# Kernel optimization log

Measured on AMD Instinct MI355X. Metric: run time of the kernel, lower is better.

Reference implementation:

```python
import jax, jax.numpy as jnp
import numpy as np

B, L, D, H = 2, 2048, 2048, 16
DH = D // H  # head dim = 128
NEG = -1e9


def setup_inputs() -> dict:
    key = jax.random.key(0)
    ks = jax.random.split(key, 8)
    scale = 1.0 / np.sqrt(D)
    x = jax.random.normal(ks[0], (B, L, D), jnp.float32)
    # causal additive mask, broadcast over batch and heads
    causal = jnp.tril(jnp.ones((L, L), jnp.float32))
    mask = jnp.where(causal == 1, 0.0, NEG)[None, None, :, :]
    # rotary tables: angle = pos / 10000^(2i/DH), tables shaped [L, DH//2]
    inv_freq = 1.0 / (10000.0 ** (jnp.arange(0, DH, 2, dtype=jnp.float32) / DH))
    ang = jnp.arange(L, dtype=jnp.float32)[:, None] * inv_freq[None, :]
    cos, sin = jnp.cos(ang), jnp.sin(ang)
    wq = jax.random.normal(ks[1], (D, D), jnp.float32) * scale
    wk = jax.random.normal(ks[2], (D, D), jnp.float32) * scale
    wv = jax.random.normal(ks[3], (D, D), jnp.float32) * scale
    wo = jax.random.normal(ks[4], (D, D), jnp.float32) * scale
    return {"x": x, "mask": mask, "cos": cos, "sin": sin,
            "wq": wq, "wk": wk, "wv": wv, "wo": wo}


def _rope(t, cos, sin):
    # t: [B, H, L, DH]; rotate interleaved pairs (Llama-style)
    t1 = t[..., 0::2]
    t2 = t[..., 1::2]
    c = cos[None, None, :, :]
    s = sin[None, None, :, :]
    out = jnp.stack([t1 * c - t2 * s, t1 * s + t2 * c], axis=-1)
    return out.reshape(t.shape)


def reference(x, mask, cos, sin, wq, wk, wv, wo):
    # nn.Linear(bias=False): y = x @ W^T, W is [out, in]
    xq = jnp.einsum('bld,ed->ble', x, wq).reshape(B, L, H, DH).transpose(0, 2, 1, 3)
    xk = jnp.einsum('bld,ed->ble', x, wk).reshape(B, L, H, DH).transpose(0, 2, 1, 3)
    xv = jnp.einsum('bld,ed->ble', x, wv).reshape(B, L, H, DH).transpose(0, 2, 1, 3)
    xq = _rope(xq, cos, sin)
    xk = _rope(xk, cos, sin)
    # no cache, num_kv_heads == num_heads (GQA branch inert in source)
    scores = jnp.einsum('bhqd,bhkd->bhqk', xq, xk) / np.sqrt(DH).astype(np.float32)
    scores = scores + mask
    probs = jax.nn.softmax(scores.astype(jnp.float32), axis=-1).astype(xq.dtype)
    out = jnp.einsum('bhqk,bhkd->bhqd', probs, xv)
    out = out.transpose(0, 2, 1, 3).reshape(B, L, H * DH)
    return jnp.einsum('ble,de->bld', out, wo)
```

## Files before the change

### kernel.cpp

```cpp
#include <hip/hip_runtime.h>
#include <math.h>

#define B 2
#define L 2048
#define D 2048
#define H 16
#define DH 128
#define M (B*L)

typedef __attribute__((ext_vector_type(8))) short bf16x8;
typedef __attribute__((ext_vector_type(4))) float f32x4;

#define GLDS(g, l) __builtin_amdgcn_global_load_lds((const __attribute__((address_space(1))) void*)(g), \
                                                    (__attribute__((address_space(3))) void*)(l), 16, 0, 0)

__device__ __forceinline__ ushort f2bf(float f) {
    union { float f; unsigned u; } v; v.f = f;
    unsigned r = v.u + 0x7fffu + ((v.u >> 16) & 1u);
    return (ushort)(r >> 16);
}
__device__ __forceinline__ float bf2f(ushort h) {
    union { unsigned u; float f; } v; v.u = ((unsigned)h) << 16;
    return v.f;
}
__device__ __forceinline__ unsigned pack2bf(float a, float b) {
    return (unsigned)f2bf(a) | ((unsigned)f2bf(b) << 16);
}
__device__ __forceinline__ unsigned pktrunc(float a, float b) {
    union { float f; unsigned u; } x, y; x.f = a; y.f = b;
    return __builtin_amdgcn_perm(y.u, x.u, 0x07060302);
}

__global__ __launch_bounds__(256) void cast_f32_to_bf16(const float* __restrict__ in,
                                                        ushort* __restrict__ out) {
    const int i = blockIdx.x * 256 + threadIdx.x;
    const float4* in4 = (const float4*)in;
    float4 a = in4[2*i], b = in4[2*i+1];
    uint4 o;
    o.x = pack2bf(a.x, a.y);  o.y = pack2bf(a.z, a.w);
    o.z = pack2bf(b.x, b.y);  o.w = pack2bf(b.z, b.w);
    ((uint4*)out)[i] = o;
}

__global__ __launch_bounds__(256) void cast4_w(const float* __restrict__ w0, const float* __restrict__ w1,
                                               const float* __restrict__ w2, const float* __restrict__ w3,
                                               ushort* o0, ushort* o1, ushort* o2, ushort* o3) {
    const int z = blockIdx.y;
    const float* src = (z == 0) ? w0 : (z == 1) ? w1 : (z == 2) ? w2 : w3;
    ushort* dst = (z == 0) ? o0 : (z == 1) ? o1 : (z == 2) ? o2 : o3;
    const int i = blockIdx.x * 256 + threadIdx.x;
    const float4* in4 = (const float4*)src;
    float4 a = in4[2*i], b = in4[2*i+1];
    uint4 o;
    o.x = pack2bf(a.x, a.y);  o.y = pack2bf(a.z, a.w);
    o.z = pack2bf(b.x, b.y);  o.w = pack2bf(b.z, b.w);
    ((uint4*)dst)[i] = o;
}

__global__ __launch_bounds__(256) void rope_bf16(ushort* __restrict__ q, ushort* __restrict__ k,
                                                 const float* __restrict__ cosp,
                                                 const float* __restrict__ sinp) {
    const int idx = blockIdx.x * 256 + threadIdx.x;
    const int i    = idx & 63;
    const int rest = idx >> 6;
    const int h    = rest & (H - 1);
    const int bl   = rest >> 4;
    const int l    = bl & (L - 1);
    const float c = cosp[l * 64 + i];
    const float s = sinp[l * 64 + i];
    const size_t base = (size_t)bl * D + h * DH + 2 * i;
    unsigned qv = *(unsigned*)(q + base);
    unsigned kv = *(unsigned*)(k + base);
    float q0 = bf2f((ushort)(qv & 0xffff)), q1 = bf2f((ushort)(qv >> 16));
    float k0 = bf2f((ushort)(kv & 0xffff)), k1 = bf2f((ushort)(kv >> 16));
    *(unsigned*)(q + base) = pack2bf(q0*c - q1*s, q0*s + q1*c);
    *(unsigned*)(k + base) = pack2bf(k0*c - k1*s, k0*s + k1*c);
}

template<bool BF16OUT>
__device__ __forceinline__ void gemm_body(const ushort* __restrict__ A,
                                          const ushort* __restrict__ Bt,
                                          void* __restrict__ Cv,
                                          int Mdim, int Ndim, int Kdim,
                                          int bx, int by) {
    __shared__ __attribute__((aligned(16))) ushort sA[4096];
    __shared__ __attribute__((aligned(16))) ushort sB[4096];
    const int tid  = threadIdx.x;
    const int lane = tid & 63, w = tid >> 6;
    const int quad = lane >> 4, l15 = lane & 15;
    const int wm = w >> 1, wn = w & 1;
    const int m0 = by * 128, n0 = bx * 128;
    const int wbase = tid & ~63;
    f32x4 acc[4][4] = {};

    for (int k0 = 0; k0 < Kdim; k0 += 32) {
#pragma unroll
        for (int i = 0; i < 2; ++i) {
            const int s = i * 256 + tid;
            const int m  = s >> 2;
            const int kc = (s & 3) ^ ((m >> 1) & 3);
            GLDS(A  + (size_t)(m0 + m) * Kdim + k0 + kc * 8, sA + (size_t)(i*256 + wbase) * 8);
            GLDS(Bt + (size_t)(n0 + m) * Kdim + k0 + kc * 8, sB + (size_t)(i*256 + wbase) * 8);
        }
        __syncthreads();
        bf16x8 af[4], bfr[4];
#pragma unroll
        for (int mt = 0; mt < 4; ++mt) {
            const int m = wm*64 + mt*16 + l15;
            const int slot = m*4 + (quad ^ ((m >> 1) & 3));
            af[mt] = *(const bf16x8*)(sA + slot*8);
        }
#pragma unroll
        for (int nt = 0; nt < 4; ++nt) {
            const int n = wn*64 + nt*16 + l15;
            const int slot = n*4 + (quad ^ ((n >> 1) & 3));
            bfr[nt] = *(const bf16x8*)(sB + slot*8);
        }
#pragma unroll
        for (int mt = 0; mt < 4; ++mt)
#pragma unroll
            for (int nt = 0; nt < 4; ++nt)
                acc[mt][nt] = __builtin_amdgcn_mfma_f32_16x16x32_bf16(af[mt], bfr[nt], acc[mt][nt], 0, 0, 0);
        __syncthreads();
    }
#pragma unroll
    for (int mt = 0; mt < 4; ++mt)
#pragma unroll
        for (int nt = 0; nt < 4; ++nt)
#pragma unroll
            for (int r = 0; r < 4; ++r) {
                const int row = m0 + wm*64 + mt*16 + quad*4 + r;
                const int col = n0 + wn*64 + nt*16 + l15;
                if (BF16OUT) ((ushort*)Cv)[(size_t)row * Ndim + col] = f2bf(acc[mt][nt][r]);
                else         ((float*) Cv)[(size_t)row * Ndim + col] = acc[mt][nt][r];
            }
}

__global__ __launch_bounds__(256) void gemm_qkv(const ushort* __restrict__ xb,
                                                const ushort* __restrict__ wq,
                                                const ushort* __restrict__ wk,
                                                const ushort* __restrict__ wv,
                                                ushort* q, ushort* k, ushort* vt) {
    const int z = blockIdx.z;
    if (z == 0)      gemm_body<true>(xb, wq, q,  M, D, D, blockIdx.x, blockIdx.y);
    else if (z == 1) gemm_body<true>(xb, wk, k,  M, D, D, blockIdx.x, blockIdx.y);
    else             gemm_body<true>(wv, xb, vt, D, M, D, blockIdx.y, blockIdx.x);
}
__global__ __launch_bounds__(256) void gemm_nt_f32(const ushort* A, const ushort* Bt, float* C,
                                                   int Mdim, int Ndim, int Kdim) {
    gemm_body<false>(A, Bt, C, Mdim, Ndim, Kdim, blockIdx.x, blockIdx.y);
}

#define SCL 0.1275174329758f

__global__ __launch_bounds__(256) void attn_lds(const ushort* __restrict__ qb,
                                                const ushort* __restrict__ kb,
                                                const ushort* __restrict__ vtb,
                                                ushort* __restrict__ ctx) {
    __shared__ __attribute__((aligned(16))) ushort sK[2][32*128];
    __shared__ __attribute__((aligned(16))) ushort sV[2][128*32];
    const int tid  = threadIdx.x;
    const int w    = tid >> 6;
    const int lane = tid & 63;
    const int quad = lane >> 4, l15 = lane & 15;
    const int wbase = tid & ~63;
    const int plane = blockIdx.x & 31;
    const int h = plane & 15, b = plane >> 4;
    const int sb = 31 - (blockIdx.x >> 5);
    const int q0 = sb * 64;
    const size_t bL = (size_t)b * L;
    const int hDH = h * DH;
    const int ntiles = 2 * (sb + 1);
    const int tmask  = sb * 2 + (w >> 1);
    const int qrow   = q0 + w * 16 + l15;

    bf16x8 qf[4];
#pragma unroll
    for (int ks = 0; ks < 4; ++ks)
        qf[ks] = *(const bf16x8*)(qb + (bL + qrow) * D + hDH + ks*32 + quad*8);

    f32x4 o[8] = {};
    float lsum = 0.0f;

    #define STAGE(buf, t) do {                                                              \
        const int k0s = (t) * 32;                                                           \
        _Pragma("unroll")                                                                   \
        for (int j = 0; j < 2; ++j) {                                                       \
            const int s = j*256 + tid;                                                      \
            const int key = s >> 4, phys = s & 15;                                          \
            const int logc = phys ^ (key & 7);                                              \
            GLDS(kb + (bL + k0s + key) * (size_t)D + hDH + logc*8,                          \
                 sK[buf] + (size_t)(j*256 + wbase) * 8);                                    \
        }                                                                                   \
        _Pragma("unroll")                                                                   \
        for (int j = 0; j < 2; ++j) {                                                       \
            const int s = j*256 + tid;                                                      \
            const int row = s >> 2, physc = s & 3;                                          \
            const int logc = physc ^ ((row >> 1) & 3);                                      \
            GLDS(vtb + (size_t)(hDH + row) * M + bL + k0s + logc*8,                         \
                 sV[buf] + (size_t)(j*256 + wbase) * 8);                                    \
        }                                                                                   \
    } while (0)

    int cur = 0;
    STAGE(0, 0);
    __syncthreads();

    for (int t = 0; t < ntiles; ++t) {
        if (t + 1 < ntiles) STAGE(cur ^ 1, t + 1);
        const ushort* sKc = sK[cur];
        const ushort* sVc = sV[cur];
        const int k0 = t * 32;

        f32x4 st[2] = {};
#pragma unroll
        for (int kt2 = 0; kt2 < 2; ++kt2)
#pragma unroll
            for (int ks = 0; ks < 4; ++ks) {
                bf16x8 kfr = *(const bf16x8*)(sKc + ((kt2*16 + l15)*16 + ((ks*4 + quad) ^ (l15 & 7)))*8);
                st[kt2] = __builtin_amdgcn_mfma_f32_16x16x32_bf16(kfr, qf[ks], st[kt2], 0, 0, 0);
            }

        const bool domask = (t >= tmask);
        unsigned pk[2][2];
        {
            float e[2][4];
#pragma unroll
            for (int kt2 = 0; kt2 < 2; ++kt2)
#pragma unroll
                for (int r = 0; r < 4; ++r) {
                    float x = exp2f(fmaf(st[kt2][r], SCL, -13.0f));
                    if (domask && (k0 + kt2*16 + quad*4 + r > qrow)) x = 0.0f;
                    e[kt2][r] = x;
                    lsum += x;
                }
#pragma unroll
            for (int kt2 = 0; kt2 < 2; ++kt2) {
                pk[kt2][0] = pktrunc(e[kt2][0], e[kt2][1]);
                pk[kt2][1] = pktrunc(e[kt2][2], e[kt2][3]);
            }
        }

        const int srcA = l15 + ((quad & 1) << 5);
        const int srcB = srcA + 16;
        const bool hi = (quad >> 1) != 0;
        {
            unsigned t00 = __shfl((int)pk[0][0], srcA), t10 = __shfl((int)pk[1][0], srcA);
            unsigned t01 = __shfl((int)pk[0][1], srcA), t11 = __shfl((int)pk[1][1], srcA);
            unsigned t02 = __shfl((int)pk[0][0], srcB), t12 = __shfl((int)pk[1][0], srcB);
            unsigned t03 = __shfl((int)pk[0][1], srcB), t13 = __shfl((int)pk[1][1], srcB);
            union { unsigned u[4]; bf16x8 v; } fr;
            fr.u[0] = hi ? t10 : t00;
            fr.u[1] = hi ? t11 : t01;
            fr.u[2] = hi ? t12 : t02;
            fr.u[3] = hi ? t13 : t13*0 + (hi ? t13 : t03);
            fr.u[3] = hi ? t13 : t03;
#pragma unroll
            for (int dt = 0; dt < 8; ++dt) {
                bf16x8 vfr = *(const bf16x8*)(sVc + ((dt*16 + l15)*4 + (quad ^ ((l15 >> 1) & 3)))*8);
                o[dt] = __builtin_amdgcn_mfma_f32_16x16x32_bf16(vfr, fr.v, o[dt], 0, 0, 0);
            }
        }

        __syncthreads();
        cur ^= 1;
    }

    {
        float v = lsum;
        v += __shfl_xor(v, 16);
        v += __shfl_xor(v, 32);
        lsum = 1.0f / v;
    }
    {
        const size_t rowb = (bL + qrow) * D + hDH;
        const float inv = lsum;
#pragma unroll
        for (int dt = 0; dt < 8; ++dt) {
            uint2 stv;
            stv.x = pktrunc(o[dt][0] * inv, o[dt][1] * inv);
            stv.y = pktrunc(o[dt][2] * inv, o[dt][3] * inv);
            *(uint2*)(ctx + rowb + dt*16 + quad*4) = stv;
        }
    }
    #undef STAGE
}

extern "C" void kernel_launch(void* const* d_in, const int* in_sizes, int n_in,
                              void* d_out, int out_size, void* d_ws, size_t ws_size,
                              hipStream_t stream) {
    (void)in_sizes; (void)n_in; (void)out_size; (void)ws_size;
    const float* x    = (const float*)d_in[0];
    const float* cosp = (const float*)d_in[2];
    const float* sinp = (const float*)d_in[3];
    const float* wq   = (const float*)d_in[4];
    const float* wk   = (const float*)d_in[5];
    const float* wv   = (const float*)d_in[6];
    const float* wo   = (const float*)d_in[7];
    float* out = (float*)d_out;

    ushort* xb  = (ushort*)d_ws;
    ushort* wqb = xb  + (size_t)M * D;
    ushort* wkb = wqb + (size_t)D * D;
    ushort* wvb = wkb + (size_t)D * D;
    ushort* wob = wvb + (size_t)D * D;
    ushort* qb2 = wob + (size_t)D * D;
    ushort* kb2 = qb2 + (size_t)M * D;
    ushort* vtb = kb2 + (size_t)M * D;
    ushort* ctxb = xb;

    cast_f32_to_bf16<<<(M*D)/2048, 256, 0, stream>>>(x, xb);
    cast4_w<<<dim3((D*D)/2048, 4), 256, 0, stream>>>(wq, wk, wv, wo, wqb, wkb, wvb, wob);

    gemm_qkv<<<dim3(16, 32, 3), 256, 0, stream>>>(xb, wqb, wkb, wvb, qb2, kb2, vtb);

    rope_bf16<<<(B*L*H*64)/256, 256, 0, stream>>>(qb2, kb2, cosp, sinp);

    attn_lds<<<dim3(32 * 32), 256, 0, stream>>>(qb2, kb2, vtb, ctxb);

    gemm_nt_f32<<<dim3(16, 32), 256, 0, stream>>>(ctxb, wob, out, M, D, D);
}
```

Measured before the change: 422.1 us.

## Rewrite projection GEMMs with 256x128 tiles, 512 threads and triple-buffered LDS

The GEMM body moves from 128x128 tiles with K-step 32 and a single LDS buffer to 256x128 tiles with K-step 64 across 8 waves. It triple-buffers LDS, issuing global-to-LDS loads two stages ahead with explicit vmcnt waits, and interleaves load issue with MFMA bursts under setprio. The goal is to hide global-memory latency, halve barrier count per K and raise data reuse per tile. The trade-off is much more LDS use (about 144KB per block), which limits occupancy to one block per CU and hardcodes K=2048.

Result: slower. 453.7 us (+7.5%).

```diff
diff --git a/kernel.cpp b/kernel.cpp
--- a/kernel.cpp
+++ b/kernel.cpp
@@ -78,77 +78,133 @@
 }
 
 template<bool BF16OUT>
-__device__ __forceinline__ void gemm_body(const ushort* __restrict__ A,
-                                          const ushort* __restrict__ Bt,
-                                          void* __restrict__ Cv,
-                                          int Mdim, int Ndim, int Kdim,
-                                          int bx, int by) {
-    __shared__ __attribute__((aligned(16))) ushort sA[4096];
-    __shared__ __attribute__((aligned(16))) ushort sB[4096];
+__device__ __forceinline__ void gemm8_body(const ushort* __restrict__ A,
+                                           const ushort* __restrict__ Bt,
+                                           void* __restrict__ Cv,
+                                           int Ndim, int bx, int by) {
+    constexpr int K  = 2048;
+    constexpr int NT = K / 64;
+    __shared__ __attribute__((aligned(16))) ushort sA[3][256*64];
+    __shared__ __attribute__((aligned(16))) ushort sB[3][128*64];
     const int tid  = threadIdx.x;
-    const int lane = tid & 63, w = tid >> 6;
+    const int lane = tid & 63;
+    const int w    = tid >> 6;
     const int quad = lane >> 4, l15 = lane & 15;
     const int wm = w >> 1, wn = w & 1;
-    const int m0 = by * 128, n0 = bx * 128;
+    const int m0 = by * 256, n0 = bx * 128;
     const int wbase = tid & ~63;
+
     f32x4 acc[4][4] = {};
 
-    for (int k0 = 0; k0 < Kdim; k0 += 32) {
-#pragma unroll
-        for (int i = 0; i < 2; ++i) {
-            const int s = i * 256 + tid;
-            const int m  = s >> 2;
-            const int kc = (s & 3) ^ ((m >> 1) & 3);
-            GLDS(A  + (size_t)(m0 + m) * Kdim + k0 + kc * 8, sA + (size_t)(i*256 + wbase) * 8);
-            GLDS(Bt + (size_t)(n0 + m) * Kdim + k0 + kc * 8, sB + (size_t)(i*256 + wbase) * 8);
-        }
-        __syncthreads();
-        bf16x8 af[4], bfr[4];
-#pragma unroll
-        for (int mt = 0; mt < 4; ++mt) {
-            const int m = wm*64 + mt*16 + l15;
-            const int slot = m*4 + (quad ^ ((m >> 1) & 3));
-            af[mt] = *(const bf16x8*)(sA + slot*8);
-        }
-#pragma unroll
-        for (int nt = 0; nt < 4; ++nt) {
-            const int n = wn*64 + nt*16 + l15;
-            const int slot = n*4 + (quad ^ ((n >> 1) & 3));
-            bfr[nt] = *(const bf16x8*)(sB + slot*8);
-        }
-#pragma unroll
-        for (int mt = 0; mt < 4; ++mt)
-#pragma unroll
-            for (int nt = 0; nt < 4; ++nt)
-                acc[mt][nt] = __builtin_amdgcn_mfma_f32_16x16x32_bf16(af[mt], bfr[nt], acc[mt][nt], 0, 0, 0);
-        __syncthreads();
+    #define STG_A(sl, kt, j) do {                                              \
+        const int s_ = (j)*512 + tid;                                          \
+        const int r_ = s_ >> 3;                                                \
+        const int lc_ = (s_ & 7) ^ (r_ & 7);                                   \
+        GLDS(A + (size_t)(m0 + r_) * K + (kt)*64 + lc_*8,                      \
+             sA[sl] + ((j)*512 + wbase) * 8);                                  \
+    } while (0)
+    #define STG_B(sl, kt, j) do {                                              \
+        const int s_ = (j)*512 + tid;                                          \
+        const int r_ = s_ >> 3;                                                \
+        const int lc_ = (s_ & 7) ^ (r_ & 7);                                   \
+        GLDS(Bt + (size_t)(n0 + r_) * K + (kt)*64 + lc_*8,                     \
+             sB[sl] + ((j)*512 + wbase) * 8);                                  \
+    } while (0)
+
+    STG_A(0,0,0); STG_A(0,0,1); STG_A(0,0,2); STG_A(0,0,3); STG_B(0,0,0); STG_B(0,0,1);
+    STG_A(1,1,0); STG_A(1,1,1); STG_A(1,1,2); STG_A(1,1,3); STG_B(1,1,0); STG_B(1,1,1);
+
+    for (int t = 0; t < NT; ++t) {
+        const int sl = t % 3;
+        const int s2 = (t + 2) % 3;
+        const ushort* sAc = sA[sl];
+        const ushort* sBc = sB[sl];
+
+        __builtin_amdgcn_s_barrier();
+        if (t + 1 < NT) { asm volatile("s_waitcnt vmcnt(6)" ::: "memory"); }
+        else            { asm volatile("s_waitcnt vmcnt(0)" ::: "memory"); }
+        __builtin_amdgcn_sched_barrier(0);
+
+        if (t + 2 < NT) { STG_A(s2, t+2, 0); STG_A(s2, t+2, 1); STG_B(s2, t+2, 0); }
+        bf16x8 bfr[4][2], af[2][2];
+#pragma unroll
+        for (int fc = 0; fc < 4; ++fc)
+#pragma unroll
+            for (int kh = 0; kh < 2; ++kh) {
+                const int r = wn*64 + fc*16 + l15;
+                const int p = (kh*4 + quad) ^ (r & 7);
+                bfr[fc][kh] = *(const bf16x8*)(sBc + (r*8 + p)*8);
+            }
+#pragma unroll
+        for (int fr = 0; fr < 2; ++fr)
+#pragma unroll
+            for (int kh = 0; kh < 2; ++kh) {
+                const int r = wm*64 + fr*16 + l15;
+                const int p = (kh*4 + quad) ^ (r & 7);
+                af[fr][kh] = *(const bf16x8*)(sAc + (r*8 + p)*8);
+            }
+        __builtin_amdgcn_s_barrier();
+        __builtin_amdgcn_s_setprio(1);
+#pragma unroll
+        for (int fr = 0; fr < 2; ++fr)
+#pragma unroll
+            for (int fc = 0; fc < 4; ++fc)
+#pragma unroll
+                for (int kh = 0; kh < 2; ++kh)
+                    acc[fr][fc] = __builtin_amdgcn_mfma_f32_16x16x32_bf16(af[fr][kh], bfr[fc][kh], acc[fr][fc], 0, 0, 0);
+        __builtin_amdgcn_s_setprio(0);
+
+        if (t + 2 < NT) { STG_A(s2, t+2, 2); STG_A(s2, t+2, 3); STG_B(s2, t+2, 1); }
+#pragma unroll
+        for (int fr = 0; fr < 2; ++fr)
+#pragma unroll
+            for (int kh = 0; kh < 2; ++kh) {
+                const int r = wm*64 + (2+fr)*16 + l15;
+                const int p = (kh*4 + quad) ^ (r & 7);
+                af[fr][kh] = *(const bf16x8*)(sAc + (r*8 + p)*8);
+            }
+        __builtin_amdgcn_s_barrier();
+        __builtin_amdgcn_s_setprio(1);
+#pragma unroll
+        for (int fr = 0; fr < 2; ++fr)
+#pragma unroll
+            for (int fc = 0; fc < 4; ++fc)
+#pragma unroll
+                for (int kh = 0; kh < 2; ++kh)
+                    acc[2+fr][fc] = __builtin_amdgcn_mfma_f32_16x16x32_bf16(af[fr][kh], bfr[fc][kh], acc[2+fr][fc], 0, 0, 0);
+        __builtin_amdgcn_s_setprio(0);
     }
-#pragma unroll
-    for (int mt = 0; mt < 4; ++mt)
-#pragma unroll
-        for (int nt = 0; nt < 4; ++nt)
+
+#pragma unroll
+    for (int fr = 0; fr < 4; ++fr)
+#pragma unroll
+        for (int fc = 0; fc < 4; ++fc)
 #pragma unroll
             for (int r = 0; r < 4; ++r) {
-                const int row = m0 + wm*64 + mt*16 + quad*4 + r;
-                const int col = n0 + wn*64 + nt*16 + l15;
-                if (BF16OUT) ((ushort*)Cv)[(size_t)row * Ndim + col] = f2bf(acc[mt][nt][r]);
-                else         ((float*) Cv)[(size_t)row * Ndim + col] = acc[mt][nt][r];
-            }
-}
-
-__global__ __launch_bounds__(256) void gemm_qkv(const ushort* __restrict__ xb,
-                                                const ushort* __restrict__ wq,
-                                                const ushort* __restrict__ wk,
-                                                const ushort* __restrict__ wv,
-                                                ushort* q, ushort* k, ushort* vt) {
-    const int z = blockIdx.z;
-    if (z == 0)      gemm_body<true>(xb, wq, q,  M, D, D, blockIdx.x, blockIdx.y);
-    else if (z == 1) gemm_body<true>(xb, wk, k,  M, D, D, blockIdx.x, blockIdx.y);
-    else             gemm_body<true>(wv, xb, vt, D, M, D, blockIdx.y, blockIdx.x);
-}
-__global__ __launch_bounds__(256) void gemm_nt_f32(const ushort* A, const ushort* Bt, float* C,
-                                                   int Mdim, int Ndim, int Kdim) {
-    gemm_body<false>(A, Bt, C, Mdim, Ndim, Kdim, blockIdx.x, blockIdx.y);
+                const int row = m0 + wm*64 + fr*16 + quad*4 + r;
+                const int col = n0 + wn*64 + fc*16 + l15;
+                if (BF16OUT) ((ushort*)Cv)[(size_t)row * Ndim + col] = f2bf(acc[fr][fc][r]);
+                else         ((float*) Cv)[(size_t)row * Ndim + col] = acc[fr][fc][r];
+            }
+    #undef STG_A
+    #undef STG_B
+}
+
+__global__ __launch_bounds__(512) void gemm_qkv8(const ushort* __restrict__ xb,
+                                                 const ushort* __restrict__ wq,
+                                                 const ushort* __restrict__ wk,
+                                                 const ushort* __restrict__ wv,
+                                                 ushort* q, ushort* k, ushort* vt) {
+    const int z = blockIdx.y;
+    const int bid = blockIdx.x;
+    if (z == 0)      gemm8_body<true>(xb, wq, q,  2048, bid & 15, bid >> 4);
+    else if (z == 1) gemm8_body<true>(xb, wk, k,  2048, bid & 15, bid >> 4);
+    else             gemm8_body<true>(wv, xb, vt, 4096, bid & 31, bid >> 5);
+}
+__global__ __launch_bounds__(512) void gemm_nt8_f32(const ushort* __restrict__ A,
+                                                    const ushort* __restrict__ Bt,
+                                                    float* __restrict__ C) {
+    gemm8_body<false>(A, Bt, C, 2048, blockIdx.x & 15, blockIdx.x >> 4);
 }
 
 #define SCL 0.1275174329758f
@@ -253,7 +309,6 @@
             fr.u[0] = hi ? t10 : t00;
             fr.u[1] = hi ? t11 : t01;
             fr.u[2] = hi ? t12 : t02;
-            fr.u[3] = hi ? t13 : t13*0 + (hi ? t13 : t03);
             fr.u[3] = hi ? t13 : t03;
 #pragma unroll
             for (int dt = 0; dt < 8; ++dt) {
@@ -312,11 +367,11 @@
     cast_f32_to_bf16<<<(M*D)/2048, 256, 0, stream>>>(x, xb);
     cast4_w<<<dim3((D*D)/2048, 4), 256, 0, stream>>>(wq, wk, wv, wo, wqb, wkb, wvb, wob);
 
-    gemm_qkv<<<dim3(16, 32, 3), 256, 0, stream>>>(xb, wqb, wkb, wvb, qb2, kb2, vtb);
+    gemm_qkv8<<<dim3(256, 3), 512, 0, stream>>>(xb, wqb, wkb, wvb, qb2, kb2, vtb);
 
     rope_bf16<<<(B*L*H*64)/256, 256, 0, stream>>>(qb2, kb2, cosp, sinp);
 
     attn_lds<<<dim3(32 * 32), 256, 0, stream>>>(qb2, kb2, vtb, ctxb);
 
-    gemm_nt_f32<<<dim3(16, 32), 256, 0, stream>>>(ctxb, wob, out, M, D, D);
-}
+    gemm_nt8_f32<<<dim3(256), 512, 0, stream>>>(ctxb, wob, out);
+}
```
